# Kernel optimization log

Measured on AMD Instinct MI355X. Metric: run time of the kernel, lower is better.

Reference implementation:

```python
import jax, jax.numpy as jnp
import numpy as np

N = 4096          # n_alive == max_neurons (all neurons alive)
IN_DIM = 784
OUT_DIM = 10
FEAT_DIM = 32
BATCH = 128
VOL = 100.0
BASE_RADIUS = 20.0


def setup_inputs() -> dict:
    key = jax.random.key(0)
    ks = jax.random.split(key, 7)
    x = jax.random.normal(ks[0], (BATCH, IN_DIM), dtype=jnp.float32)
    positions = jax.random.uniform(ks[1], (N, 3), dtype=jnp.float32) * VOL
    input_weights = jax.random.normal(ks[2], (N, IN_DIM), dtype=jnp.float32) * 0.1
    features = jax.random.normal(ks[3], (N, FEAT_DIM), dtype=jnp.float32) * 0.1
    output_weights = jax.random.normal(ks[4], (N, OUT_DIM), dtype=jnp.float32) * 0.1
    connection_radii = jnp.ones((N,), dtype=jnp.float32) * BASE_RADIUS
    thresholds = jnp.zeros((N,), dtype=jnp.float32)
    return {
        "x": x,
        "positions": positions,
        "input_weights": input_weights,
        "features": features,
        "output_weights": output_weights,
        "connection_radii": connection_radii,
        "thresholds": thresholds,
        "n_iterations": 2,
    }


def reference(x, positions, input_weights, features, output_weights,
              connection_radii, thresholds, n_iterations):
    # clamp positions into the volume (per-axis, same bounds since cube)
    pos = jnp.clip(positions, 0.1, VOL - 0.1)          # [N,3]
    radii = jnp.clip(connection_radii, 1.0, 50.0)      # [N]

    # pairwise Euclidean distances (cdist)
    diff = pos[:, None, :] - pos[None, :, :]           # [N,N,3]
    dist = jnp.sqrt(jnp.maximum(jnp.sum(diff * diff, axis=-1), 1e-12))  # [N,N]

    max_radius = jnp.max(radii)
    connection_mask = dist < max_radius                # [N,N] bool

    # exp-decay attenuation, clamped exponent, masked by radius graph
    atten = jnp.exp(-jnp.minimum(dist / (radii[:, None] + 1e-6), 20.0))
    atten = atten * connection_mask.astype(atten.dtype)

    # cosine feature similarity (F.normalize with eps)
    feat_norm = features / jnp.maximum(
        jnp.linalg.norm(features, axis=1, keepdims=True), 1e-6)
    feat_sim = feat_norm @ feat_norm.T                 # [N,N]

    conn_weights = atten * (0.3 + 0.7 * jnp.clip(feat_sim, -1.0, 1.0))
    conn_weights = conn_weights / (jnp.sum(conn_weights, axis=1, keepdims=True) + 1e-6)

    # spatial input/output gating along x axis
    x_coords = jnp.clip(pos[:, 0] / VOL, 0.0, 1.0)     # [N]
    input_weight = jnp.exp(-3.0 * x_coords)
    input_weight = input_weight / (jnp.sum(input_weight) + 1e-6)

    activations = (x @ input_weights.T) * input_weight  # [B,N]

    for _ in range(n_iterations):
        aggregated = activations @ conn_weights.T       # [B,N]
        activations = jax.nn.relu(activations + aggregated - thresholds)
        activations = jnp.minimum(activations, 100.0)

    output_weight = jnp.exp(3.0 * (x_coords - 1.0))
    output_weight = output_weight / (jnp.sum(output_weight) + 1e-6)
    weighted_output = output_weights * output_weight[:, None]  # [N,OUT]
    return activations @ weighted_output                # [B,OUT]
```

## Files before the change

### kernel.cpp

```cpp
#include <hip/hip_runtime.h>

#define NN 4096
#define BB 128
#define IND 784
#define FD 32
#define OD 10
#define CAP 512
#define HCAP 384

#define OFF_PART   0
#define OFF_ROWSUM 64
#define OFF_CNT    4160
#define OFF_PR4    8256
#define OFF_FNORM  24640
#define OFF_IWN    155712
#define OFF_OWT    159808
#define OFF_ACTA   163904
#define OFF_ACTB   688192
#define OFF_COLW   1212480
#define OFF_COLI   3309632

__device__ __forceinline__ int fsw(int row, int kq) {
  return row * 8 + ((kq + (row & 7)) & 7);
}

__global__ __launch_bounds__(256) void k_prep(
    const float* __restrict__ positions, const float* __restrict__ radii,
    const float* __restrict__ features, float* __restrict__ ws,
    float* __restrict__ out) {
  const int tid = threadIdx.x, bid = blockIdx.x;
  const int i = bid * 256 + tid;

  float px = fminf(fmaxf(positions[i*3+0], 0.1f), 99.9f);
  float py = fminf(fmaxf(positions[i*3+1], 0.1f), 99.9f);
  float pz = fminf(fmaxf(positions[i*3+2], 0.1f), 99.9f);
  float rc = fminf(fmaxf(radii[i], 1.0f), 50.0f);
  ((float4*)(ws + OFF_PR4))[i] = make_float4(px, py, pz, rc);

  float xc = fminf(fmaxf(px / 100.0f, 0.0f), 1.0f);
  float ew = expf(-3.0f * xc);
  float eo = expf(3.0f * (xc - 1.0f));
  ws[OFF_IWN + i] = ew;
  ws[OFF_OWT + i] = eo;

  ws[OFF_ROWSUM + i] = 0.f;
  ((int*)ws)[OFF_CNT + i] = 0;
  if (bid == 0) {
    for (int o = tid; o < BB * OD; o += 256) out[o] = 0.f;
  }

  const float4* f4 = (const float4*)(features + (size_t)i * FD);
  float4 fr[8];
  float n2 = 0.f;
  #pragma unroll
  for (int q = 0; q < 8; q++) {
    fr[q] = f4[q];
    n2 += fr[q].x*fr[q].x + fr[q].y*fr[q].y + fr[q].z*fr[q].z + fr[q].w*fr[q].w;
  }
  float inv = 1.0f / fmaxf(sqrtf(n2), 1e-6f);
  float4* o4 = (float4*)(ws + OFF_FNORM + (size_t)i * FD);
  #pragma unroll
  for (int q = 0; q < 8; q++) {
    float4 v = fr[q];
    v.x *= inv; v.y *= inv; v.z *= inv; v.w *= inv;
    o4[q] = v;
  }

  __shared__ float red[256];
  red[tid] = ew; __syncthreads();
  for (int s = 128; s > 0; s >>= 1) { if (tid < s) red[tid] += red[tid+s]; __syncthreads(); }
  if (tid == 0) ws[OFF_PART + bid] = red[0];
  __syncthreads();
  red[tid] = eo; __syncthreads();
  for (int s = 128; s > 0; s >>= 1) { if (tid < s) red[tid] += red[tid+s]; __syncthreads(); }
  if (tid == 0) ws[OFF_PART + 16 + bid] = red[0];
  __syncthreads();
  red[tid] = rc; __syncthreads();
  for (int s = 128; s > 0; s >>= 1) { if (tid < s) red[tid] = fmaxf(red[tid], red[tid+s]); __syncthreads(); }
  if (tid == 0) ws[OFF_PART + 32 + bid] = red[0];
}

__global__ __launch_bounds__(256) void k_build(float* __restrict__ ws) {
  __shared__ float4 fnI4[64*8];
  __shared__ float4 fnJ4[64*8];
  __shared__ float4 pPI[64];
  __shared__ float pJx[64], pJy[64], pJz[64];
  __shared__ float srow[64];
  __shared__ unsigned int hpack[HCAP];
  __shared__ float hdist[HCAP];
  __shared__ int rcnt[64];
  __shared__ int rbase[64];
  __shared__ int nhit;

  const int tid = threadIdx.x;
  const int i0 = blockIdx.x * 64, j0 = blockIdx.y * 64;
  const float* fnorm = ws + OFF_FNORM;
  const float4* pr4 = (const float4*)(ws + OFF_PR4);

  for (int v = tid; v < 512; v += 256) {
    int row = v >> 3, kq = v & 7;
    fnI4[fsw(row, kq)] = *(const float4*)&fnorm[(size_t)(i0+row)*FD + kq*4];
    fnJ4[fsw(row, kq)] = *(const float4*)&fnorm[(size_t)(j0+row)*FD + kq*4];
  }
  if (tid < 64) {
    pPI[tid] = pr4[i0 + tid];
    srow[tid] = 0.f;
    rcnt[tid] = 0;
  } else if (tid < 128) {
    int t = tid - 64;
    float4 pj = pr4[j0 + t];
    pJx[t] = pj.x; pJy[t] = pj.y; pJz[t] = pj.z;
  }
  if (tid == 0) nhit = 0;

  float maxrad = ws[OFF_PART + 32];
  #pragma unroll
  for (int p = 1; p < 16; p++) maxrad = fmaxf(maxrad, ws[OFF_PART + 32 + p]);
  __syncthreads();

  const int tx = tid & 15, ty = tid >> 4;
  float4 pif[4];
  #pragma unroll
  for (int r = 0; r < 4; r++) pif[r] = pPI[ty*4 + r];
  float pjx[4], pjy[4], pjz[4];
  #pragma unroll
  for (int c = 0; c < 4; c++) { int jl = tx*4+c; pjx[c]=pJx[jl]; pjy[c]=pJy[jl]; pjz[c]=pJz[jl]; }

  #pragma unroll
  for (int r = 0; r < 4; r++) {
    const int il = ty*4 + r;
    #pragma unroll
    for (int c = 0; c < 4; c++) {
      const int jl = tx*4 + c;
      float dx = pif[r].x - pjx[c], dy = pif[r].y - pjy[c], dz = pif[r].z - pjz[c];
      float d2 = fmaf(dx, dx, fmaf(dy, dy, dz*dz));
      float dist = sqrtf(fmaxf(d2, 1e-12f));
      if (dist < maxrad) {
        int h = atomicAdd(&nhit, 1);
        if (h < HCAP) {
          hpack[h] = (unsigned)(il | (jl << 6));
          hdist[h] = dist;
        }
      }
    }
  }
  __syncthreads();

  const int nh = min(nhit, HCAP);

  for (int h = tid; h < nh; h += 256) {
    unsigned pk = hpack[h];
    int il = pk & 63, jl = (pk >> 6) & 63;
    float4 pi = pPI[il];
    float dist = hdist[h];
    float t = fminf(dist / (pi.w + 1e-6f), 20.0f);
    float at = expf(-t);
    float s = 0.f;
    #pragma unroll
    for (int kq = 0; kq < 8; kq++) {
      float4 a = fnI4[fsw(il, kq)];
      float4 b = fnJ4[fsw(jl, kq)];
      s = fmaf(a.x, b.x, s); s = fmaf(a.y, b.y, s);
      s = fmaf(a.z, b.z, s); s = fmaf(a.w, b.w, s);
    }
    s = fminf(fmaxf(s, -1.f), 1.f);
    float wv = at * fmaf(0.7f, s, 0.3f);
    int ls = atomicAdd(&rcnt[il], 1);
    hpack[h] = (unsigned)(il | (jl << 6) | (ls << 12));
    hdist[h] = wv;
    atomicAdd(&srow[il], wv);
  }
  __syncthreads();

  if (tid < 64) {
    int c = rcnt[tid];
    rbase[tid] = (c > 0) ? atomicAdd(&((int*)ws)[OFF_CNT + i0 + tid], c) : 0;
    atomicAdd(&ws[OFF_ROWSUM + i0 + tid], srow[tid]);
  }
  __syncthreads();

  int* coli = (int*)(ws + OFF_COLI);
  float* colw = ws + OFF_COLW;
  for (int h = tid; h < nh; h += 256) {
    unsigned pk = hpack[h];
    int il = pk & 63, jl = (pk >> 6) & 63, ls = (int)(pk >> 12);
    int slot = rbase[il] + ls;
    if (slot < CAP) {
      size_t off = (size_t)(i0 + il) * CAP + slot;
      coli[off] = j0 + jl;
      colw[off] = hdist[h];
    }
  }
}

__global__ __launch_bounds__(256) void k_fc1(
    const float* __restrict__ x, const float* __restrict__ W, float* __restrict__ ws) {
  __shared__ float Wt[64*20];
  __shared__ float xt[32*20];
  const int tid = threadIdx.x;
  const int b0 = blockIdx.x * 32, i0 = blockIdx.y * 64;
  const int tx = tid & 15, ty = tid >> 4;

  float siw = 0.f;
  #pragma unroll
  for (int p = 0; p < 16; p++) siw += ws[OFF_PART + p];
  const float ginv = 1.0f / (siw + 1e-6f);

  float acc[4][2] = {};
  for (int k0 = 0; k0 < IND; k0 += 16) {
    __syncthreads();
    {
      int row = tid >> 2, kq = tid & 3;
      *(float4*)&Wt[row*20 + kq*4] = *(const float4*)&W[(size_t)(i0+row)*IND + k0 + kq*4];
      if (tid < 128) {
        int rb = tid >> 2, kq2 = tid & 3;
        *(float4*)&xt[rb*20 + kq2*4] = *(const float4*)&x[(size_t)(b0+rb)*IND + k0 + kq2*4];
      }
    }
    __syncthreads();
    #pragma unroll
    for (int k4 = 0; k4 < 4; k4++) {
      float4 A[4], Bv[2];
      #pragma unroll
      for (int r = 0; r < 4; r++) A[r]  = *(const float4*)&Wt[(ty*4+r)*20 + k4*4];
      #pragma unroll
      for (int c = 0; c < 2; c++) Bv[c] = *(const float4*)&xt[(tx + c*16)*20 + k4*4];
      #pragma unroll
      for (int r = 0; r < 4; r++)
        #pragma unroll
        for (int c = 0; c < 2; c++) {
          acc[r][c] = fmaf(A[r].x, Bv[c].x, acc[r][c]);
          acc[r][c] = fmaf(A[r].y, Bv[c].y, acc[r][c]);
          acc[r][c] = fmaf(A[r].z, Bv[c].z, acc[r][c]);
          acc[r][c] = fmaf(A[r].w, Bv[c].w, acc[r][c]);
        }
    }
  }
  #pragma unroll
  for (int r = 0; r < 4; r++) {
    int i = i0 + ty*4 + r;
    float g = ws[OFF_IWN + i] * ginv;
    #pragma unroll
    for (int c = 0; c < 2; c++)
      ws[OFF_ACTA + (size_t)i*BB + b0 + tx + c*16] = acc[r][c] * g;
  }
}

__global__ __launch_bounds__(256) void k_agg(
    const float* __restrict__ actIn, float* __restrict__ actOut,
    const int* __restrict__ coli, const float* __restrict__ colw,
    const int* __restrict__ cnt, const float* __restrict__ rowsum,
    const float* __restrict__ thr) {
  const int tid = threadIdx.x;
  const int i = blockIdx.x*2 + (tid >> 7);
  const int b = tid & 127;
  int nn = cnt[i]; nn = nn < CAP ? nn : CAP;
  const int*   ci = coli + (size_t)i*CAP;
  const float* cw = colw + (size_t)i*CAP;
  float acc = 0.f;
  int s = 0;
  for (; s + 4 <= nn; s += 4) {
    int j0 = ci[s], j1 = ci[s+1], j2 = ci[s+2], j3 = ci[s+3];
    float w0 = cw[s], w1 = cw[s+1], w2 = cw[s+2], w3 = cw[s+3];
    float a0 = actIn[(size_t)j0*BB + b];
    float a1 = actIn[(size_t)j1*BB + b];
    float a2 = actIn[(size_t)j2*BB + b];
    float a3 = actIn[(size_t)j3*BB + b];
    acc = fmaf(a0, w0, acc); acc = fmaf(a1, w1, acc);
    acc = fmaf(a2, w2, acc); acc = fmaf(a3, w3, acc);
  }
  for (; s < nn; s++) acc = fmaf(actIn[(size_t)ci[s]*BB + b], cw[s], acc);
  float agg = acc / (rowsum[i] + 1e-6f);
  float v = actIn[(size_t)i*BB + b] + agg - thr[i];
  v = fminf(fmaxf(v, 0.f), 100.f);
  actOut[(size_t)i*BB + b] = v;
}

__global__ __launch_bounds__(128) void k_out(
    const float* __restrict__ act, const float* __restrict__ wraw,
    const float* __restrict__ ws, float* __restrict__ out) {
  const int b = threadIdx.x;
  const int i0 = blockIdx.x * 128;
  float sow = 0.f;
  #pragma unroll
  for (int p = 0; p < 16; p++) sow += ws[OFF_PART + 16 + p];
  const float inv = 1.0f / (sow + 1e-6f);
  float acc[OD] = {};
  for (int ii = 0; ii < 128; ii++) {
    int i = i0 + ii;
    float aw = act[(size_t)i*BB + b] * (ws[OFF_OWT + i] * inv);
    #pragma unroll
    for (int o = 0; o < OD; o++) acc[o] = fmaf(aw, wraw[i*OD + o], acc[o]);
  }
  #pragma unroll
  for (int o = 0; o < OD; o++) atomicAdd(&out[b*OD + o], acc[o]);
}

extern "C" void kernel_launch(void* const* d_in, const int* in_sizes, int n_in,
                              void* d_out, int out_size, void* d_ws, size_t ws_size,
                              hipStream_t stream) {
  const float* x              = (const float*)d_in[0];
  const float* positions      = (const float*)d_in[1];
  const float* input_weights  = (const float*)d_in[2];
  const float* features       = (const float*)d_in[3];
  const float* output_weights = (const float*)d_in[4];
  const float* radii          = (const float*)d_in[5];
  const float* thresholds     = (const float*)d_in[6];

  float* ws  = (float*)d_ws;
  float* out = (float*)d_out;

  k_prep<<<16, 256, 0, stream>>>(positions, radii, features, ws, out);
  k_build<<<dim3(64, 64), 256, 0, stream>>>(ws);
  k_fc1<<<dim3(4, 64), 256, 0, stream>>>(x, input_weights, ws);

  float* actA = ws + OFF_ACTA;
  float* actB = ws + OFF_ACTB;
  const int* cnt  = (const int*)(ws + OFF_CNT);
  const int* coli = (const int*)(ws + OFF_COLI);

  k_agg<<<NN/2, 256, 0, stream>>>(actA, actB, coli, ws + OFF_COLW, cnt, ws + OFF_ROWSUM, thresholds);
  k_agg<<<NN/2, 256, 0, stream>>>(actB, actA, coli, ws + OFF_COLW, cnt, ws + OFF_ROWSUM, thresholds);

  k_out<<<NN/128, 128, 0, stream>>>(actA, output_weights, ws, out);
}
```

Baseline: 233.2 us.

## Double-buffer fc1 shared tiles and halve batch tile to double grid size

The input-projection GEMM kernel now prefetches the next K-slice of weights and inputs into registers while computing on the current shared-memory buffer, using two shared buffers and a single barrier per step. The batch tile shrinks from 32 to 16, so the grid grows from 256 to 512 blocks to better fill the GPU's compute units. Each block now reloads the same weight tile twice as often across batch tiles, and each thread holds fewer accumulators, which lowers arithmetic intensity per shared-memory load.

```diff
diff --git a/kernel.cpp b/kernel.cpp
--- a/kernel.cpp
+++ b/kernel.cpp
@@ -195,54 +195,62 @@
 
 __global__ __launch_bounds__(256) void k_fc1(
     const float* __restrict__ x, const float* __restrict__ W, float* __restrict__ ws) {
-  __shared__ float Wt[64*20];
-  __shared__ float xt[32*20];
+  __shared__ float Wt[2][64*20];
+  __shared__ float xt[2][16*20];
   const int tid = threadIdx.x;
-  const int b0 = blockIdx.x * 32, i0 = blockIdx.y * 64;
-  const int tx = tid & 15, ty = tid >> 4;
+  const int d = blockIdx.x;
+  const int bx = d >> 6;
+  const int by = d & 63;
+  const int b0 = bx * 16, i0 = by * 64;
+  const int tx = tid & 15;
+  const int ty = tid >> 4;
+  const int row = tid >> 2, q = tid & 3;
+
+  *(float4*)&Wt[0][row*20 + q*4] = *(const float4*)&W[(size_t)(i0+row)*IND + q*4];
+  if (tid < 64)
+    *(float4*)&xt[0][(tid>>2)*20 + q*4] = *(const float4*)&x[(size_t)(b0+(tid>>2))*IND + q*4];
+  __syncthreads();
+
+  float acc[4] = {0.f, 0.f, 0.f, 0.f};
+
+  for (int step = 0; step < 49; step++) {
+    const int cur = step & 1;
+    float4 wreg, xreg;
+    const bool pf = (step + 1 < 49);
+    if (pf) {
+      const int k0 = (step + 1) * 16;
+      wreg = *(const float4*)&W[(size_t)(i0+row)*IND + k0 + q*4];
+      if (tid < 64)
+        xreg = *(const float4*)&x[(size_t)(b0+(tid>>2))*IND + k0 + q*4];
+    }
+    #pragma unroll
+    for (int kq = 0; kq < 4; kq++) {
+      float4 Bv = *(const float4*)&xt[cur][tx*20 + kq*4];
+      #pragma unroll
+      for (int r = 0; r < 4; r++) {
+        float4 A = *(const float4*)&Wt[cur][(ty*4+r)*20 + kq*4];
+        acc[r] = fmaf(A.x, Bv.x, acc[r]);
+        acc[r] = fmaf(A.y, Bv.y, acc[r]);
+        acc[r] = fmaf(A.z, Bv.z, acc[r]);
+        acc[r] = fmaf(A.w, Bv.w, acc[r]);
+      }
+    }
+    if (pf) {
+      *(float4*)&Wt[cur^1][row*20 + q*4] = wreg;
+      if (tid < 64) *(float4*)&xt[cur^1][(tid>>2)*20 + q*4] = xreg;
+    }
+    __syncthreads();
+  }
 
   float siw = 0.f;
   #pragma unroll
   for (int p = 0; p < 16; p++) siw += ws[OFF_PART + p];
   const float ginv = 1.0f / (siw + 1e-6f);
 
-  float acc[4][2] = {};
-  for (int k0 = 0; k0 < IND; k0 += 16) {
-    __syncthreads();
-    {
-      int row = tid >> 2, kq = tid & 3;
-      *(float4*)&Wt[row*20 + kq*4] = *(const float4*)&W[(size_t)(i0+row)*IND + k0 + kq*4];
-      if (tid < 128) {
-        int rb = tid >> 2, kq2 = tid & 3;
-        *(float4*)&xt[rb*20 + kq2*4] = *(const float4*)&x[(size_t)(b0+rb)*IND + k0 + kq2*4];
-      }
-    }
-    __syncthreads();
-    #pragma unroll
-    for (int k4 = 0; k4 < 4; k4++) {
-      float4 A[4], Bv[2];
-      #pragma unroll
-      for (int r = 0; r < 4; r++) A[r]  = *(const float4*)&Wt[(ty*4+r)*20 + k4*4];
-      #pragma unroll
-      for (int c = 0; c < 2; c++) Bv[c] = *(const float4*)&xt[(tx + c*16)*20 + k4*4];
-      #pragma unroll
-      for (int r = 0; r < 4; r++)
-        #pragma unroll
-        for (int c = 0; c < 2; c++) {
-          acc[r][c] = fmaf(A[r].x, Bv[c].x, acc[r][c]);
-          acc[r][c] = fmaf(A[r].y, Bv[c].y, acc[r][c]);
-          acc[r][c] = fmaf(A[r].z, Bv[c].z, acc[r][c]);
-          acc[r][c] = fmaf(A[r].w, Bv[c].w, acc[r][c]);
-        }
-    }
-  }
   #pragma unroll
   for (int r = 0; r < 4; r++) {
-    int i = i0 + ty*4 + r;
-    float g = ws[OFF_IWN + i] * ginv;
-    #pragma unroll
-    for (int c = 0; c < 2; c++)
-      ws[OFF_ACTA + (size_t)i*BB + b0 + tx + c*16] = acc[r][c] * g;
+    const int i = i0 + ty*4 + r;
+    ws[OFF_ACTA + (size_t)i*BB + b0 + tx] = acc[r] * (ws[OFF_IWN + i] * ginv);
   }
 }
 
@@ -312,7 +320,7 @@
 
   k_prep<<<16, 256, 0, stream>>>(positions, radii, features, ws, out);
   k_build<<<dim3(64, 64), 256, 0, stream>>>(ws);
-  k_fc1<<<dim3(4, 64), 256, 0, stream>>>(x, input_weights, ws);
+  k_fc1<<<512, 256, 0, stream>>>(x, input_weights, ws);
 
   float* actA = ws + OFF_ACTA;
   float* actB = ws + OFF_ACTB;
```

New measurement: 210.6 us. 9.7% less time.

## Replace tiled LDS fc1 GEMM with direct-load per-thread dot products; widen k_out grid

Applied to the files above, without the earlier changes.

The shared-memory tiled fc1 kernel is replaced by one where each thread owns a batch index and computes four neuron dot products. The weight rows are wave-uniform loads via readfirstlane, and the x rows are read straight from global/L1 with no LDS staging or barriers. The grid grows from 256 to 512 blocks. Separately, k_out now has each block process 32 neurons instead of 128, giving 128 blocks to raise parallelism at the cost of more atomics. The risk is that fc1 loses its register tiling reuse: every thread re-reads a full 784-float x row per block, which puts more pressure on the caches.

```diff
diff --git a/kernel.cpp b/kernel.cpp
--- a/kernel.cpp
+++ b/kernel.cpp
@@ -195,55 +195,41 @@
 
 __global__ __launch_bounds__(256) void k_fc1(
     const float* __restrict__ x, const float* __restrict__ W, float* __restrict__ ws) {
-  __shared__ float Wt[64*20];
-  __shared__ float xt[32*20];
   const int tid = threadIdx.x;
-  const int b0 = blockIdx.x * 32, i0 = blockIdx.y * 64;
-  const int tx = tid & 15, ty = tid >> 4;
+  const int b = tid & 127;
+  const int iset = tid >> 7;
+  const int iu = __builtin_amdgcn_readfirstlane((int)(blockIdx.x * 8) + iset * 4);
+
+  const float4* xr = (const float4*)(x + (size_t)b * IND);
+  const float4* w0 = (const float4*)(W + (size_t)(iu + 0) * IND);
+  const float4* w1 = (const float4*)(W + (size_t)(iu + 1) * IND);
+  const float4* w2 = (const float4*)(W + (size_t)(iu + 2) * IND);
+  const float4* w3 = (const float4*)(W + (size_t)(iu + 3) * IND);
+
+  float a0 = 0.f, a1 = 0.f, a2 = 0.f, a3 = 0.f;
+  #pragma unroll 4
+  for (int kc = 0; kc < IND/4; kc++) {
+    float4 xv = xr[kc];
+    float4 v0 = w0[kc], v1 = w1[kc], v2 = w2[kc], v3 = w3[kc];
+    a0 = fmaf(xv.x, v0.x, a0); a0 = fmaf(xv.y, v0.y, a0);
+    a0 = fmaf(xv.z, v0.z, a0); a0 = fmaf(xv.w, v0.w, a0);
+    a1 = fmaf(xv.x, v1.x, a1); a1 = fmaf(xv.y, v1.y, a1);
+    a1 = fmaf(xv.z, v1.z, a1); a1 = fmaf(xv.w, v1.w, a1);
+    a2 = fmaf(xv.x, v2.x, a2); a2 = fmaf(xv.y, v2.y, a2);
+    a2 = fmaf(xv.z, v2.z, a2); a2 = fmaf(xv.w, v2.w, a2);
+    a3 = fmaf(xv.x, v3.x, a3); a3 = fmaf(xv.y, v3.y, a3);
+    a3 = fmaf(xv.z, v3.z, a3); a3 = fmaf(xv.w, v3.w, a3);
+  }
 
   float siw = 0.f;
   #pragma unroll
   for (int p = 0; p < 16; p++) siw += ws[OFF_PART + p];
   const float ginv = 1.0f / (siw + 1e-6f);
 
-  float acc[4][2] = {};
-  for (int k0 = 0; k0 < IND; k0 += 16) {
-    __syncthreads();
-    {
-      int row = tid >> 2, kq = tid & 3;
-      *(float4*)&Wt[row*20 + kq*4] = *(const float4*)&W[(size_t)(i0+row)*IND + k0 + kq*4];
-      if (tid < 128) {
-        int rb = tid >> 2, kq2 = tid & 3;
-        *(float4*)&xt[rb*20 + kq2*4] = *(const float4*)&x[(size_t)(b0+rb)*IND + k0 + kq2*4];
-      }
-    }
-    __syncthreads();
-    #pragma unroll
-    for (int k4 = 0; k4 < 4; k4++) {
-      float4 A[4], Bv[2];
-      #pragma unroll
-      for (int r = 0; r < 4; r++) A[r]  = *(const float4*)&Wt[(ty*4+r)*20 + k4*4];
-      #pragma unroll
-      for (int c = 0; c < 2; c++) Bv[c] = *(const float4*)&xt[(tx + c*16)*20 + k4*4];
-      #pragma unroll
-      for (int r = 0; r < 4; r++)
-        #pragma unroll
-        for (int c = 0; c < 2; c++) {
-          acc[r][c] = fmaf(A[r].x, Bv[c].x, acc[r][c]);
-          acc[r][c] = fmaf(A[r].y, Bv[c].y, acc[r][c]);
-          acc[r][c] = fmaf(A[r].z, Bv[c].z, acc[r][c]);
-          acc[r][c] = fmaf(A[r].w, Bv[c].w, acc[r][c]);
-        }
-    }
-  }
-  #pragma unroll
-  for (int r = 0; r < 4; r++) {
-    int i = i0 + ty*4 + r;
-    float g = ws[OFF_IWN + i] * ginv;
-    #pragma unroll
-    for (int c = 0; c < 2; c++)
-      ws[OFF_ACTA + (size_t)i*BB + b0 + tx + c*16] = acc[r][c] * g;
-  }
+  ws[OFF_ACTA + (size_t)(iu+0)*BB + b] = a0 * (ws[OFF_IWN + iu+0] * ginv);
+  ws[OFF_ACTA + (size_t)(iu+1)*BB + b] = a1 * (ws[OFF_IWN + iu+1] * ginv);
+  ws[OFF_ACTA + (size_t)(iu+2)*BB + b] = a2 * (ws[OFF_IWN + iu+2] * ginv);
+  ws[OFF_ACTA + (size_t)(iu+3)*BB + b] = a3 * (ws[OFF_IWN + iu+3] * ginv);
 }
 
 __global__ __launch_bounds__(256) void k_agg(
@@ -280,13 +266,13 @@
     const float* __restrict__ act, const float* __restrict__ wraw,
     const float* __restrict__ ws, float* __restrict__ out) {
   const int b = threadIdx.x;
-  const int i0 = blockIdx.x * 128;
+  const int i0 = blockIdx.x * 32;
   float sow = 0.f;
   #pragma unroll
   for (int p = 0; p < 16; p++) sow += ws[OFF_PART + 16 + p];
   const float inv = 1.0f / (sow + 1e-6f);
   float acc[OD] = {};
-  for (int ii = 0; ii < 128; ii++) {
+  for (int ii = 0; ii < 32; ii++) {
     int i = i0 + ii;
     float aw = act[(size_t)i*BB + b] * (ws[OFF_OWT + i] * inv);
     #pragma unroll
@@ -312,7 +298,7 @@
 
   k_prep<<<16, 256, 0, stream>>>(positions, radii, features, ws, out);
   k_build<<<dim3(64, 64), 256, 0, stream>>>(ws);
-  k_fc1<<<dim3(4, 64), 256, 0, stream>>>(x, input_weights, ws);
+  k_fc1<<<NN/8, 256, 0, stream>>>(x, input_weights, ws);
 
   float* actA = ws + OFF_ACTA;
   float* actB = ws + OFF_ACTB;
@@ -322,5 +308,5 @@
   k_agg<<<NN/2, 256, 0, stream>>>(actA, actB, coli, ws + OFF_COLW, cnt, ws + OFF_ROWSUM, thresholds);
   k_agg<<<NN/2, 256, 0, stream>>>(actB, actA, coli, ws + OFF_COLW, cnt, ws + OFF_ROWSUM, thresholds);
 
-  k_out<<<NN/128, 128, 0, stream>>>(actA, output_weights, ws, out);
-}
+  k_out<<<NN/32, 128, 0, stream>>>(actA, output_weights, ws, out);
+}
```

Measured after the change: 230.5 us. About the same (-1.2%).
